# Performance work log

Hardware: AMD Instinct MI355X
Metric: run time of the kernel (lower is better)

The kernel has to match this reference:

```python
import jax, jax.numpy as jnp
import numpy as np

H = W = 128
R = 2
H2, W2 = H // R, W // R
TOPK = 3
NSEG = H * W + 1  # segment 0 = background


def _ccl(binary):
    """8-connected component labeling via iterative max-label propagation.
    binary: [H,W] bool. Returns int32 labels, 0 = background; each component
    gets a unique (arbitrary) positive id = max pixel index in the component."""
    idx = jnp.arange(1, H * W + 1, dtype=jnp.int32).reshape(H, W)
    lab0 = jnp.where(binary, idx, 0)

    def cond(c):
        return c[1]

    def body(c):
        lab, _ = c
        nb = jax.lax.reduce_window(lab, jnp.int32(0), jax.lax.max,
                                   (3, 3), (1, 1), 'SAME')  # 3x3 incl. self
        new = jnp.where(binary, nb, 0)
        return new, jnp.any(new != lab)

    lab, _ = jax.lax.while_loop(cond, body, (lab0, jnp.bool_(True)))
    return lab


def _process_one(prob_i, feat_i):
    """prob_i: [1,H,W], feat_i: [Cf,H,W] -> [3*Cf, H2, W2]."""
    p = prob_i[0]
    binary = p > 0.5
    lab = _ccl(binary).reshape(-1)  # [H*W] segment ids

    ones = jnp.ones((H * W,), jnp.float32)
    count = jax.ops.segment_sum(ones, lab, num_segments=NSEG)
    conf_sum = jax.ops.segment_sum(p.reshape(-1), lab, num_segments=NSEG)
    mean_conf = conf_sum / jnp.maximum(count, 1.0)

    rows = jnp.repeat(jnp.arange(H, dtype=jnp.int32), W)
    cols = jnp.tile(jnp.arange(W, dtype=jnp.int32), H)
    min_r = jax.ops.segment_min(rows, lab, num_segments=NSEG)
    max_r = jax.ops.segment_max(rows, lab, num_segments=NSEG)
    min_c = jax.ops.segment_min(cols, lab, num_segments=NSEG)
    max_c = jax.ops.segment_max(cols, lab, num_segments=NSEG)

    valid = (count > 0) & (jnp.arange(NSEG) > 0)
    score = jnp.where(valid, mean_conf, -jnp.inf)
    _, top_idx = jax.lax.top_k(score, TOPK)  # regions sorted by mean confidence
    K = jnp.sum(valid.astype(jnp.int32))     # number of connected regions

    # duplication rules: K==0 -> full image x3; K==1 -> [f0,f0,f0];
    # K==2 -> [f0,f0,f1]; K>=3 -> [f0,f1,f2]
    i0, i1 = top_idx[0], top_idx[1]
    slots = jnp.where(K >= 3, top_idx,
            jnp.where(K == 2, jnp.stack([i0, i0, i1]),
                      jnp.stack([i0, i0, i0])))

    mr = jnp.where(K > 0, min_r[slots], 0)
    Mr = jnp.where(K > 0, max_r[slots] + 1, H)  # bbox half-open, regionprops style
    mc = jnp.where(K > 0, min_c[slots], 0)
    Mc = jnp.where(K > 0, max_c[slots] + 1, W)

    def crop(a, b, c, d):
        # PyTorch nearest interpolate: src = floor(dst * in/out)
        r = a + (jnp.arange(H2) * (b - a)) // H2
        cc = c + (jnp.arange(W2) * (d - c)) // W2
        return feat_i[:, r][:, :, cc]  # [Cf, H2, W2]

    out = jax.vmap(crop)(mr, Mr, mc, Mc)  # [3, Cf, H2, W2]
    return out.reshape(-1, H2, W2)         # [3*Cf, H2, W2]


def setup_inputs() -> dict:
    key = jax.random.key(0)
    k1, k2 = jax.random.split(key)
    prob = jax.random.uniform(k1, (16, 1, H, W), dtype=jnp.float32)
    feat = jax.random.normal(k2, (16, 192, H, W), dtype=jnp.float32)
    return {"prob": prob, "feat": feat}


def reference(prob, feat):
    return jax.vmap(_process_one)(prob, feat)  # [B, 3*Cf, H2, W2]
```

## Files before the change

kernel.cpp:

```cpp
#include <hip/hip_runtime.h>
#include <limits.h>

#define HH 128
#define WW_ 128
#define HW 16384
#define NB 16
#define CF 192
#define H2 64
#define W2 64
#define NRUN 8192
#define NCOMP 4096

typedef float vf4 __attribute__((ext_vector_type(4)));
typedef unsigned long long ull;


__device__ inline int uf_find(int* par, int x) {
    volatile int* vp = (volatile int*)par;
    int p = vp[x];
    while (p != x) {
        int g = vp[p];
        vp[x] = g;
        x = g;
        p = vp[x];
    }
    return x;
}

__device__ inline void uf_union(int* par, int a, int b) {
    int ra = uf_find(par, a);
    int rb = uf_find(par, b);
    while (ra != rb) {
        if (ra < rb) { int t = ra; ra = rb; rb = t; }
        int old = atomicCAS(&par[ra], ra, rb);
        if (old == ra) return;
        ra = uf_find(par, old);
        rb = uf_find(par, rb);
    }
}


__device__ inline int getbit2(ull lo, ull hi, int c) {
    return (int)(((c < 64) ? (lo >> c) : (hi >> (c - 64))) & 1ULL);
}

__device__ inline int leading_ones(ull v) {
    ull nv = ~v;
    return (nv == 0ULL) ? 64 : __clzll(nv);
}

__device__ inline int trailing_ones(ull v) {
    ull nv = ~v;
    return (nv == 0ULL) ? 64 : (__ffsll(nv) - 1);
}

__device__ inline int run_start_col(ull lo, ull hi, int c) {
    if (c < 64) {
        int ones = leading_ones(lo << (63 - c));
        return c - ones + 1;
    }
    int ones = leading_ones(hi << (127 - c));
    int rs = c - ones + 1;
    if (rs == 64) rs -= leading_ones(lo);
    return rs;
}

__device__ inline int run_end_col(ull lo, ull hi, int c) {
    if (c >= 64) {
        return c + trailing_ones(hi >> (c - 64)) - 1;
    }
    int e = c + trailing_ones(lo >> c) - 1;
    if (e == 63) e += trailing_ones(hi);
    return e;
}

__device__ inline int run_index(ull rs_lo, ull rs_hi, int cs) {
    if (cs < 64)  return __popcll(rs_lo & ((1ULL << cs) - 1ULL));
    if (cs == 64) return __popcll(rs_lo);
    return __popcll(rs_lo) + __popcll(rs_hi & ((1ULL << (cs - 64)) - 1ULL));
}

__device__ inline void top3_ins(float s, int id, int x,
    float& s0, float& s1, float& s2,
    int& i0, int& i1, int& i2,
    int& x0, int& x1, int& x2)
{
    if (x < 0) return;
    if (s > s0 || (s == s0 && id < i0)) {
        s2 = s1; i2 = i1; x2 = x1;
        s1 = s0; i1 = i0; x1 = x0;
        s0 = s;  i0 = id; x0 = x;
    } else if (s > s1 || (s == s1 && id < i1)) {
        s2 = s1; i2 = i1; x2 = x1;
        s1 = s;  i1 = id; x1 = x;
    } else if (s > s2 || (s == s2 && id < i2)) {
        s2 = s;  i2 = id; x2 = x;
    }
}


__global__ __launch_bounds__(1024) void ccl_kernel(
    const float* __restrict__ prob, int* __restrict__ bbox)
{
    __shared__ int parent[NRUN];
    __shared__ ull rowmask[HH][2];
    __shared__ int   lcnt[NCOMP];
    __shared__ float lconf[NCOMP];
    __shared__ int lminr[NCOMP], lmaxr[NCOMP];
    __shared__ int lminc[NCOMP], lmaxc[NCOMP];
    __shared__ int lmaxid[NCOMP];
    __shared__ int snroots;
    __shared__ float wss[48];
    __shared__ int wid_[48], wrx[48];

    const int b = blockIdx.x;
    const int tid = threadIdx.x;
    const float* p = prob + (size_t)b * HW;

    if (tid == 0) snroots = 0;

    #pragma unroll
    for (int k = 0; k < HW / 1024; ++k) {
        int i = k * 1024 + tid;
        ull m = __ballot(p[i] > 0.5f);
        if ((tid & 63) == 0) rowmask[i >> 7][(i >> 6) & 1] = m;
    }
    for (int j = tid; j < NCOMP; j += 1024) {
        lcnt[j] = 0; lconf[j] = 0.f;
        lminr[j] = INT_MAX; lmaxr[j] = -1;
        lminc[j] = INT_MAX; lmaxc[j] = -1;
        lmaxid[j] = 0;
    }
    __syncthreads();

    for (int rid = tid; rid < NRUN; rid += 1024) {
        int r = rid >> 6;
        ull lo = rowmask[r][0], hi = rowmask[r][1];
        ull rs_lo = lo & ~(lo << 1);
        ull rs_hi = hi & ~((hi << 1) | (lo >> 63));
        int nruns = __popcll(rs_lo) + __popcll(rs_hi);
        if ((rid & 63) < nruns) parent[rid] = rid;
    }
    __syncthreads();

    for (int k = 0; k < HW / 1024; ++k) {
        int i = k * 1024 + tid;
        int r = i >> 7, c = i & 127;
        if (r == 0) continue;
        ull lo = rowmask[r][0], hi = rowmask[r][1];
        if (!getbit2(lo, hi, c)) continue;
        ull ulo = rowmask[r - 1][0], uhi = rowmask[r - 1][1];
        int l  = (c > 0)   ? getbit2(lo, hi, c - 1) : 0;
        int rt = (c < 127) ? getbit2(lo, hi, c + 1) : 0;
        int up = getbit2(ulo, uhi, c);
        int ul = (c > 0)   ? getbit2(ulo, uhi, c - 1) : 0;
        int ur = (c < 127) ? getbit2(ulo, uhi, c + 1) : 0;
        bool u1 = up && !(l && ul);
        bool u2 = !up && ul && !l;
        bool u3 = !up && ur && !rt;
        if (!(u1 | u2 | u3)) continue;
        ull rs_lo = lo & ~(lo << 1),   rs_hi = hi & ~((hi << 1) | (lo >> 63));
        ull urs_lo = ulo & ~(ulo << 1), urs_hi = uhi & ~((uhi << 1) | (ulo >> 63));
        int cs = run_start_col(lo, hi, c);
        int rid = (r << 6) + run_index(rs_lo, rs_hi, cs);
        int ub = (r - 1) << 6;
        if (u1) uf_union(parent, rid, ub + run_index(urs_lo, urs_hi, run_start_col(ulo, uhi, c)));
        if (u2) uf_union(parent, rid, ub + run_index(urs_lo, urs_hi, run_start_col(ulo, uhi, c - 1)));
        if (u3) uf_union(parent, rid, ub + run_index(urs_lo, urs_hi, run_start_col(ulo, uhi, c + 1)));
    }
    __syncthreads();

    for (int rid = tid; rid < NRUN; rid += 1024) {
        int r = rid >> 6;
        ull lo = rowmask[r][0], hi = rowmask[r][1];
        ull rs_lo = lo & ~(lo << 1);
        ull rs_hi = hi & ~((hi << 1) | (lo >> 63));
        int nruns = __popcll(rs_lo) + __popcll(rs_hi);
        if ((rid & 63) < nruns) parent[rid] = uf_find(parent, rid);
    }
    __syncthreads();
    for (int rid = tid; rid < NRUN; rid += 1024) {
        int r = rid >> 6;
        ull lo = rowmask[r][0], hi = rowmask[r][1];
        ull rs_lo = lo & ~(lo << 1);
        ull rs_hi = hi & ~((hi << 1) | (lo >> 63));
        int nruns = __popcll(rs_lo) + __popcll(rs_hi);
        if ((rid & 63) < nruns && parent[rid] == rid) {
            int idx = atomicAdd(&snroots, 1);
            parent[rid] = NRUN + idx;
        }
    }
    __syncthreads();

    {
        int row = tid >> 3;
        int w0 = (tid & 7) * 16;
        ull lo = rowmask[row][0], hi = rowmask[row][1];
        ull rs_lo = lo & ~(lo << 1);
        ull rs_hi = hi & ~((hi << 1) | (lo >> 63));
        ull seg = ((w0 < 64) ? (rs_lo >> w0) : (rs_hi >> (w0 - 64))) & 0xFFFFULL;
        int curIdx = -1, aCnt = 0, aMinc = 0, aMaxc = 0, aMaxid = 0;
        float aConf = 0.f;
        while (seg) {
            int c = w0 + (__ffsll(seg) - 1);
            seg &= seg - 1;
            int e = run_end_col(lo, hi, c);
            int rid = (row << 6) + run_index(rs_lo, rs_hi, c);
            int v = parent[rid];
            int idx = (v >= NRUN) ? (v - NRUN) : (parent[v] - NRUN);
            float s = 0.f;
            for (int j = c; j <= e; ++j) s += p[(row << 7) + j];
            if (idx == curIdx) {
                aCnt += e - c + 1; aConf += s;
                aMaxc = e; aMaxid = (row << 7) + e + 1;
            } else {
                if (curIdx >= 0) {
                    atomicAdd(&lcnt[curIdx], aCnt);
                    atomicAdd(&lconf[curIdx], aConf);
                    atomicMin(&lminr[curIdx], row);
                    atomicMax(&lmaxr[curIdx], row);
                    atomicMin(&lminc[curIdx], aMinc);
                    atomicMax(&lmaxc[curIdx], aMaxc);
                    atomicMax(&lmaxid[curIdx], aMaxid);
                }
                curIdx = idx; aCnt = e - c + 1; aConf = s;
                aMinc = c; aMaxc = e; aMaxid = (row << 7) + e + 1;
            }
        }
        if (curIdx >= 0) {
            atomicAdd(&lcnt[curIdx], aCnt);
            atomicAdd(&lconf[curIdx], aConf);
            atomicMin(&lminr[curIdx], row);
            atomicMax(&lmaxr[curIdx], row);
            atomicMin(&lminc[curIdx], aMinc);
            atomicMax(&lmaxc[curIdx], aMaxc);
            atomicMax(&lmaxid[curIdx], aMaxid);
        }
    }
    __syncthreads();

    const int n = snroots;
    float s0 = -INFINITY, s1 = -INFINITY, s2 = -INFINITY;
    int i0 = INT_MAX, i1 = INT_MAX, i2 = INT_MAX;
    int x0 = -1, x1 = -1, x2 = -1;
    for (int j = tid; j < n; j += 1024) {
        float s = lconf[j] / (float)lcnt[j];
        top3_ins(s, lmaxid[j], j, s0, s1, s2, i0, i1, i2, x0, x1, x2);
    }
    for (int off = 32; off; off >>= 1) {
        float bs0 = __shfl_xor(s0, off), bs1 = __shfl_xor(s1, off), bs2 = __shfl_xor(s2, off);
        int bi0 = __shfl_xor(i0, off), bi1 = __shfl_xor(i1, off), bi2 = __shfl_xor(i2, off);
        int bx0 = __shfl_xor(x0, off), bx1 = __shfl_xor(x1, off), bx2 = __shfl_xor(x2, off);
        top3_ins(bs0, bi0, bx0, s0, s1, s2, i0, i1, i2, x0, x1, x2);
        top3_ins(bs1, bi1, bx1, s0, s1, s2, i0, i1, i2, x0, x1, x2);
        top3_ins(bs2, bi2, bx2, s0, s1, s2, i0, i1, i2, x0, x1, x2);
    }
    if ((tid & 63) == 0) {
        int w = tid >> 6;
        wss[w * 3 + 0] = s0; wid_[w * 3 + 0] = i0; wrx[w * 3 + 0] = x0;
        wss[w * 3 + 1] = s1; wid_[w * 3 + 1] = i1; wrx[w * 3 + 1] = x1;
        wss[w * 3 + 2] = s2; wid_[w * 3 + 2] = i2; wrx[w * 3 + 2] = x2;
    }
    __syncthreads();

    if (tid == 0) {
        float t0 = -INFINITY, t1 = -INFINITY, t2 = -INFINITY;
        int ti0 = INT_MAX, ti1 = INT_MAX, ti2 = INT_MAX;
        int tx0 = -1, tx1 = -1, tx2 = -1;
        for (int t = 0; t < 48; ++t)
            top3_ins(wss[t], wid_[t], wrx[t], t0, t1, t2, ti0, ti1, ti2, tx0, tx1, tx2);
        int K = n;
        int roots[3];
        if (K >= 3)      { roots[0] = tx0; roots[1] = tx1; roots[2] = tx2; }
        else if (K == 2) { roots[0] = tx0; roots[1] = tx0; roots[2] = tx1; }
        else             { roots[0] = tx0; roots[1] = tx0; roots[2] = tx0; }
        for (int slot = 0; slot < 3; ++slot) {
            int mr, h, mc, w;
            if (K == 0) { mr = 0; h = HH; mc = 0; w = WW_; }
            else {
                int rt = roots[slot];
                mr = lminr[rt]; h = lmaxr[rt] + 1 - mr;
                mc = lminc[rt]; w = lmaxc[rt] + 1 - mc;
            }
            int* o = bbox + (b * 3 + slot) * 4;
            o[0] = mr; o[1] = h; o[2] = mc; o[3] = w;
        }
    }
}


__global__ __launch_bounds__(256) void crop_kernel(
    const float* __restrict__ feat, const int* __restrict__ bbox,
    float* __restrict__ out)
{
    const int gid = blockIdx.x * 256 + threadIdx.x;
    const int x4 = gid & 15;
    const int y  = (gid >> 4) & 63;
    const int t  = gid >> 10;
    const int c  = t % CF;
    const int bs = t / CF;
    const int* bb = bbox + bs * 4;
    const int mr = bb[0], h = bb[1], mc = bb[2], w = bb[3];
    const int r = mr + ((y * h) >> 6);
    const int bimg = bs / 3;
    const float* row = feat + (((size_t)bimg * CF + c) * HH + r) * WW_;
    const int x = x4 * 4;
    vf4 v;
    v.x = row[mc + (((x + 0) * w) >> 6)];
    v.y = row[mc + (((x + 1) * w) >> 6)];
    v.z = row[mc + (((x + 2) * w) >> 6)];
    v.w = row[mc + (((x + 3) * w) >> 6)];
    __builtin_nontemporal_store(v, (vf4*)out + gid);
}


extern "C" void kernel_launch(void* const* d_in, const int* in_sizes, int n_in,
                              void* d_out, int out_size, void* d_ws, size_t ws_size,
                              hipStream_t stream) {
    const float* prob = (const float*)d_in[0];
    const float* feat = (const float*)d_in[1];
    float* out = (float*)d_out;

    int* bbox = (int*)d_ws;

    hipLaunchKernelGGL(ccl_kernel, dim3(NB), dim3(1024), 0, stream,
                       prob, bbox);
    const int total4 = NB * 3 * CF * H2 * (W2 / 4);
    hipLaunchKernelGGL(crop_kernel, dim3(total4 / 256), dim3(256), 0, stream,
                       feat, bbox, out);
}
```

Before: 386.4 us.

## Merge run unions hierarchically by row strides to cut union-find contention

Replaces the single all-pixel union pass with a log-depth hierarchical merge. At stride s, only boundary rows s*(2k+1) union with the row above, and each step ends with a full path-compression pass. It also precomputes per-row run-start masks and run counts in shared memory, so later passes reuse them instead of recomputing. The aim is to reduce long union-find chains and atomic contention, at the cost of seven compression passes and extra barriers.

```diff
diff --git a/kernel.cpp b/kernel.cpp
--- a/kernel.cpp
+++ b/kernel.cpp
@@ -104,6 +104,8 @@
 {
     __shared__ int parent[NRUN];
     __shared__ ull rowmask[HH][2];
+    __shared__ ull rsmask[HH][2];
+    __shared__ int nrunrow[HH];
     __shared__ int   lcnt[NCOMP];
     __shared__ float lconf[NCOMP];
     __shared__ int lminr[NCOMP], lmaxr[NCOMP];
@@ -133,59 +135,52 @@
     }
     __syncthreads();
 
-    for (int rid = tid; rid < NRUN; rid += 1024) {
-        int r = rid >> 6;
+    for (int r = tid; r < HH; r += 1024) {
         ull lo = rowmask[r][0], hi = rowmask[r][1];
         ull rs_lo = lo & ~(lo << 1);
         ull rs_hi = hi & ~((hi << 1) | (lo >> 63));
-        int nruns = __popcll(rs_lo) + __popcll(rs_hi);
-        if ((rid & 63) < nruns) parent[rid] = rid;
-    }
-    __syncthreads();
-
-    for (int k = 0; k < HW / 1024; ++k) {
-        int i = k * 1024 + tid;
-        int r = i >> 7, c = i & 127;
-        if (r == 0) continue;
-        ull lo = rowmask[r][0], hi = rowmask[r][1];
-        if (!getbit2(lo, hi, c)) continue;
-        ull ulo = rowmask[r - 1][0], uhi = rowmask[r - 1][1];
-        int l  = (c > 0)   ? getbit2(lo, hi, c - 1) : 0;
-        int rt = (c < 127) ? getbit2(lo, hi, c + 1) : 0;
-        int up = getbit2(ulo, uhi, c);
-        int ul = (c > 0)   ? getbit2(ulo, uhi, c - 1) : 0;
-        int ur = (c < 127) ? getbit2(ulo, uhi, c + 1) : 0;
-        bool u1 = up && !(l && ul);
-        bool u2 = !up && ul && !l;
-        bool u3 = !up && ur && !rt;
-        if (!(u1 | u2 | u3)) continue;
-        ull rs_lo = lo & ~(lo << 1),   rs_hi = hi & ~((hi << 1) | (lo >> 63));
-        ull urs_lo = ulo & ~(ulo << 1), urs_hi = uhi & ~((uhi << 1) | (ulo >> 63));
-        int cs = run_start_col(lo, hi, c);
-        int rid = (r << 6) + run_index(rs_lo, rs_hi, cs);
-        int ub = (r - 1) << 6;
-        if (u1) uf_union(parent, rid, ub + run_index(urs_lo, urs_hi, run_start_col(ulo, uhi, c)));
-        if (u2) uf_union(parent, rid, ub + run_index(urs_lo, urs_hi, run_start_col(ulo, uhi, c - 1)));
-        if (u3) uf_union(parent, rid, ub + run_index(urs_lo, urs_hi, run_start_col(ulo, uhi, c + 1)));
-    }
-    __syncthreads();
+        rsmask[r][0] = rs_lo; rsmask[r][1] = rs_hi;
+        nrunrow[r] = __popcll(rs_lo) + __popcll(rs_hi);
+    }
+    __syncthreads();
+
+    for (int rid = tid; rid < NRUN; rid += 1024)
+        if ((rid & 63) < nrunrow[rid >> 6]) parent[rid] = rid;
+    __syncthreads();
+
+    for (int s = 1; s <= 64; s <<= 1) {
+        const int items = (64 / s) * WW_;
+        for (int it = tid; it < items; it += 1024) {
+            int k = it >> 7, c = it & 127;
+            int r = s * (2 * k + 1);
+            ull lo = rowmask[r][0], hi = rowmask[r][1];
+            if (!getbit2(lo, hi, c)) continue;
+            ull ulo = rowmask[r - 1][0], uhi = rowmask[r - 1][1];
+            int l  = (c > 0)   ? getbit2(lo, hi, c - 1) : 0;
+            int rt = (c < 127) ? getbit2(lo, hi, c + 1) : 0;
+            int up = getbit2(ulo, uhi, c);
+            int ul = (c > 0)   ? getbit2(ulo, uhi, c - 1) : 0;
+            int ur = (c < 127) ? getbit2(ulo, uhi, c + 1) : 0;
+            bool u1 = up && !(l && ul);
+            bool u2 = !up && ul && !l;
+            bool u3 = !up && ur && !rt;
+            if (!(u1 | u2 | u3)) continue;
+            ull rs_lo = rsmask[r][0], rs_hi = rsmask[r][1];
+            ull urs_lo = rsmask[r - 1][0], urs_hi = rsmask[r - 1][1];
+            int rid = (r << 6) + run_index(rs_lo, rs_hi, run_start_col(lo, hi, c));
+            int ub = (r - 1) << 6;
+            if (u1) uf_union(parent, rid, ub + run_index(urs_lo, urs_hi, run_start_col(ulo, uhi, c)));
+            if (u2) uf_union(parent, rid, ub + run_index(urs_lo, urs_hi, run_start_col(ulo, uhi, c - 1)));
+            if (u3) uf_union(parent, rid, ub + run_index(urs_lo, urs_hi, run_start_col(ulo, uhi, c + 1)));
+        }
+        __syncthreads();
+        for (int rid = tid; rid < NRUN; rid += 1024)
+            if ((rid & 63) < nrunrow[rid >> 6]) parent[rid] = uf_find(parent, rid);
+        __syncthreads();
+    }
 
     for (int rid = tid; rid < NRUN; rid += 1024) {
-        int r = rid >> 6;
-        ull lo = rowmask[r][0], hi = rowmask[r][1];
-        ull rs_lo = lo & ~(lo << 1);
-        ull rs_hi = hi & ~((hi << 1) | (lo >> 63));
-        int nruns = __popcll(rs_lo) + __popcll(rs_hi);
-        if ((rid & 63) < nruns) parent[rid] = uf_find(parent, rid);
-    }
-    __syncthreads();
-    for (int rid = tid; rid < NRUN; rid += 1024) {
-        int r = rid >> 6;
-        ull lo = rowmask[r][0], hi = rowmask[r][1];
-        ull rs_lo = lo & ~(lo << 1);
-        ull rs_hi = hi & ~((hi << 1) | (lo >> 63));
-        int nruns = __popcll(rs_lo) + __popcll(rs_hi);
-        if ((rid & 63) < nruns && parent[rid] == rid) {
+        if ((rid & 63) < nrunrow[rid >> 6] && parent[rid] == rid) {
             int idx = atomicAdd(&snroots, 1);
             parent[rid] = NRUN + idx;
         }
@@ -196,8 +191,7 @@
         int row = tid >> 3;
         int w0 = (tid & 7) * 16;
         ull lo = rowmask[row][0], hi = rowmask[row][1];
-        ull rs_lo = lo & ~(lo << 1);
-        ull rs_hi = hi & ~((hi << 1) | (lo >> 63));
+        ull rs_lo = rsmask[row][0], rs_hi = rsmask[row][1];
         ull seg = ((w0 < 64) ? (rs_lo >> w0) : (rs_hi >> (w0 - 64))) & 0xFFFFULL;
         int curIdx = -1, aCnt = 0, aMinc = 0, aMaxc = 0, aMaxid = 0;
         float aConf = 0.f;
```

After: 399.9 us. 3.5% more time.
